# Kernel optimization log

Measured on AMD Instinct MI355X. Metric: run time of the kernel, lower is better.

Reference implementation:

```python
import jax, jax.numpy as jnp
import numpy as np

TOP_K = 2

def _sparse_moe(x, gate_w, w1, w2, w3):
    # x: [b, S, D] -> per-token top-k routed SwiGLU experts (Mixtral style)
    D = x.shape[-1]
    E = gate_w.shape[1]
    t = x.reshape(-1, D)                      # [T, D] tokens
    logits = t @ gate_w                       # [T, E]
    probs = jax.nn.softmax(logits, axis=-1)
    topw, topi = jax.lax.top_k(probs, TOP_K)  # [T, k]
    topw = topw / jnp.sum(topw, axis=-1, keepdims=True)
    out = jnp.zeros_like(t)
    for e in range(E):  # small fixed expert loop
        w_e = jnp.sum(jnp.where(topi == e, topw, 0.0), axis=-1)  # [T]
        h = jax.nn.silu(t @ w1[e]) * (t @ w3[e])                 # [T, F]
        out = out + (h @ w2[e]) * w_e[:, None]
    return out.reshape(x.shape)

def setup_inputs() -> dict:
    key = jax.random.key(0)
    ks = jax.random.split(key, 5)
    B, S, D, F, E = 4, 512, 1024, 4096, 8
    sc = 0.02
    return {
        "data": jax.random.normal(ks[0], (B, S, D), jnp.float32),
        "gate_w": jax.random.normal(ks[1], (D, E), jnp.float32) * sc,
        "w1": jax.random.normal(ks[2], (E, D, F), jnp.float32) * sc,
        "w2": jax.random.normal(ks[3], (E, F, D), jnp.float32) * sc,
        "w3": jax.random.normal(ks[4], (E, D, F), jnp.float32) * sc,
    }

def reference(data, gate_w, w1, w2, w3):
    # FeedForward._mixlora_forward: slice batch per lora config, run MoE,
    # combine with index_add_ (disjoint ranges covering the batch).
    B = data.shape[0]
    splits = [(0, B // 2), (B // 2, B)]  # two lora_batch_data_config_ entries
    final = jnp.zeros_like(data)
    for s, e in splits:
        y = _sparse_moe(data[s:e], gate_w, w1, w2, w3)
        final = final.at[jnp.arange(s, e)].add(y)  # index_add_ combine
    return final
```

## Files before the change

kernel.cpp:

```cpp
#include <hip/hip_runtime.h>
#include <hip/hip_bf16.h>
#include <math.h>

#define D_DIM 1024
#define F_DIM 4096
#define N_EXP 8

typedef __attribute__((ext_vector_type(4))) float f32x4;
typedef __attribute__((ext_vector_type(8))) short bf16x8;

__device__ __forceinline__ unsigned short f2bf(float f) {
    union { float f; unsigned int u; } v; v.f = f;
    unsigned int r = v.u + 0x7fffu + ((v.u >> 16) & 1u);
    return (unsigned short)(r >> 16);
}

#define GLDS16(g, l) __builtin_amdgcn_global_load_lds( \
    (const __attribute__((address_space(1))) void*)(g), \
    (__attribute__((address_space(3))) void*)(l), 16, 0, 0)

#define WAIT12_BAR asm volatile("s_waitcnt vmcnt(12)\ns_barrier" ::: "memory")
#define WAIT9_BAR  asm volatile("s_waitcnt vmcnt(9)\ns_barrier" ::: "memory")
#define BAR        asm volatile("s_barrier" ::: "memory")
#define DRAIN      asm volatile("s_waitcnt vmcnt(0)" ::: "memory")

__global__ void cast_x_kernel(const float* __restrict__ x, unsigned short* __restrict__ xb, int n4) {
    int i = blockIdx.x * blockDim.x + threadIdx.x;
    if (i >= n4) return;
    float4 v = ((const float4*)x)[i];
    unsigned int lo = (unsigned int)f2bf(v.x) | ((unsigned int)f2bf(v.y) << 16);
    unsigned int hi = (unsigned int)f2bf(v.z) | ((unsigned int)f2bf(v.w) << 16);
    ((uint2*)xb)[i] = make_uint2(lo, hi);
}

__global__ __launch_bounds__(256) void transpose_cast_kernel(
    const float* __restrict__ in, unsigned short* __restrict__ out, int R, int C) {
    __shared__ float tile[64][65];
    int e = blockIdx.x & 7;
    const float* inp = in + (size_t)e * R * C;
    unsigned short* outp = out + (size_t)e * R * C;
    int r0 = blockIdx.y * 64, c0 = (blockIdx.x >> 3) * 64;
    int tid = threadIdx.x;
    int tr = tid >> 4, tc = (tid & 15) * 4;
#pragma unroll
    for (int i = 0; i < 4; i++) {
        float4 v = *(const float4*)(inp + (size_t)(r0 + tr + i * 16) * C + c0 + tc);
        tile[tr + i * 16][tc + 0] = v.x;
        tile[tr + i * 16][tc + 1] = v.y;
        tile[tr + i * 16][tc + 2] = v.z;
        tile[tr + i * 16][tc + 3] = v.w;
    }
    __syncthreads();
    int wc = tid >> 4, wr = (tid & 15) * 4;
#pragma unroll
    for (int i = 0; i < 4; i++) {
        int c = wc + i * 16;
        ushort4 o;
        o.x = f2bf(tile[wr + 0][c]);
        o.y = f2bf(tile[wr + 1][c]);
        o.z = f2bf(tile[wr + 2][c]);
        o.w = f2bf(tile[wr + 3][c]);
        *(ushort4*)(outp + (size_t)(c0 + c) * R + r0 + wr) = o;
    }
}

__global__ void gate_kernel(const float* __restrict__ x, const float* __restrict__ gw,
                            int* __restrict__ counts, int* __restrict__ perm,
                            float* __restrict__ wts, int* __restrict__ islot, int T) {
    int wid = threadIdx.x >> 6, lane = threadIdx.x & 63;
    int token = blockIdx.x * 4 + wid;
    if (token >= T) return;
    float acc[N_EXP];
#pragma unroll
    for (int e = 0; e < N_EXP; e++) acc[e] = 0.f;
    const float* xr = x + (size_t)token * D_DIM;
    for (int i = 0; i < D_DIM / 64; i++) {
        int d = lane + 64 * i;
        float v = xr[d];
#pragma unroll
        for (int e = 0; e < N_EXP; e++) acc[e] += v * gw[d * N_EXP + e];
    }
#pragma unroll
    for (int off = 32; off >= 1; off >>= 1) {
#pragma unroll
        for (int e = 0; e < N_EXP; e++) acc[e] += __shfl_xor(acc[e], off, 64);
    }
    if (lane == 0) {
        float m = acc[0];
#pragma unroll
        for (int e = 1; e < N_EXP; e++) m = fmaxf(m, acc[e]);
        float p[N_EXP];
#pragma unroll
        for (int e = 0; e < N_EXP; e++) p[e] = expf(acc[e] - m);
        int a = 0;
        for (int e = 1; e < N_EXP; e++) if (p[e] > p[a]) a = e;
        int b = (a == 0) ? 1 : 0;
        for (int e = 0; e < N_EXP; e++) if (e != a && p[e] > p[b]) b = e;
        float s = p[a] + p[b];
        int pa = atomicAdd(&counts[a], 1);
        perm[(size_t)a * T + pa] = token; wts[(size_t)a * T + pa] = p[a] / s;
        int pb = atomicAdd(&counts[b], 1);
        perm[(size_t)b * T + pb] = token; wts[(size_t)b * T + pb] = p[b] / s;
        islot[2 * token + 0] = a * T + pa;
        islot[2 * token + 1] = b * T + pb;
    }
}

__global__ void offsets_kernel(const int* __restrict__ counts, int* __restrict__ offs) {
    if (threadIdx.x == 0 && blockIdx.x == 0) {
        int s = 0;
        for (int e = 0; e < N_EXP; e++) { offs[e] = s; s += counts[e]; }
        offs[N_EXP] = s;
    }
}

__global__ __launch_bounds__(256, 4) void gemm1_kernel(
    const unsigned short* __restrict__ xb, const unsigned short* __restrict__ w1t,
    const unsigned short* __restrict__ w3t, const int* __restrict__ counts,
    const int* __restrict__ offs, const int* __restrict__ perm,
    unsigned short* __restrict__ hbuf, int T)
{
    int bid = blockIdx.x;
    int s  = bid & 7;
    int rt = (bid >> 3) & 15;
    int ce = ((bid >> 7) << 3) | s;
    int e  = ce & 7;
    int ct = ce >> 3;
    int n_e = counts[e];
    int row0 = rt * 128;
    if (row0 >= n_e) return;
    int c0 = ct * 64;
    const unsigned short* w1e = w1t + (size_t)e * F_DIM * D_DIM;
    const unsigned short* w3e = w3t + (size_t)e * F_DIM * D_DIM;
    __shared__ __attribute__((aligned(16))) unsigned short As[4][4096];
    __shared__ __attribute__((aligned(16))) unsigned short B1s[4][2048];
    __shared__ __attribute__((aligned(16))) unsigned short B3s[4][2048];
    int tid = threadIdx.x;
    int wid = tid >> 6, lane = tid & 63;
    int wm = wid >> 1, wn = wid & 1;
    int q = lane >> 4, ln = lane & 15;

    int sr = tid >> 2, sc = tid & 3;
    int q0 = sc ^ ((sr >> 1) & 3);
    int tok0 = perm[(size_t)e * T + min(row0 + sr, n_e - 1)];
    int tok1 = perm[(size_t)e * T + min(row0 + sr + 64, n_e - 1)];
    const unsigned short* ag0 = xb + (size_t)tok0 * D_DIM + q0 * 8;
    const unsigned short* ag1 = xb + (size_t)tok1 * D_DIM + q0 * 8;
    const unsigned short* b1g = w1e + (size_t)(c0 + sr) * D_DIM + q0 * 8;
    const unsigned short* b3g = w3e + (size_t)(c0 + sr) * D_DIM + q0 * 8;
    int wo = wid * 512;

    int a_off[4], b_off[2];
#pragma unroll
    for (int i = 0; i < 4; i++) {
        int m = wm * 64 + i * 16 + ln;
        a_off[i] = m * 32 + (q ^ ((m >> 1) & 3)) * 8;
    }
#pragma unroll
    for (int j = 0; j < 2; j++) {
        int n = wn * 32 + j * 16 + ln;
        b_off[j] = n * 32 + (q ^ ((n >> 1) & 3)) * 8;
    }

    f32x4 acc1[4][2], acc3[4][2];
#pragma unroll
    for (int i = 0; i < 4; i++)
#pragma unroll
        for (int j = 0; j < 2; j++) {
            acc1[i][j] = (f32x4){0.f, 0.f, 0.f, 0.f};
            acc3[i][j] = (f32x4){0.f, 0.f, 0.f, 0.f};
        }

#define ISSUE1(B, K) do { \
    GLDS16(ag0 + (K), &As[B][wo]); \
    GLDS16(ag1 + (K), &As[B][wo + 2048]); \
    GLDS16(b1g + (K), &B1s[B][wo]); \
    GLDS16(b3g + (K), &B3s[B][wo]); } while (0)

#define COMPUTE1(B) do { \
    bf16x8 af[4]; \
    _Pragma("unroll") for (int i = 0; i < 4; i++) af[i] = *(const bf16x8*)&As[B][a_off[i]]; \
    _Pragma("unroll") for (int j = 0; j < 2; j++) { \
        bf16x8 b1f = *(const bf16x8*)&B1s[B][b_off[j]]; \
        bf16x8 b3f = *(const bf16x8*)&B3s[B][b_off[j]]; \
        _Pragma("unroll") for (int i = 0; i < 4; i++) { \
            acc1[i][j] = __builtin_amdgcn_mfma_f32_16x16x32_bf16(af[i], b1f, acc1[i][j], 0, 0, 0); \
            acc3[i][j] = __builtin_amdgcn_mfma_f32_16x16x32_bf16(af[i], b3f, acc3[i][j], 0, 0, 0); \
        } \
    } } while (0)

    ISSUE1(0, 0);
    ISSUE1(1, 32);
    ISSUE1(2, 64);
    for (int it = 0; it < 32; it += 4) {
        int k3 = it + 3, k4 = it + 4, k5 = it + 5, k6 = it + 6;
        ISSUE1(3, (k3 < 32) ? k3 * 32 : 0);
        WAIT12_BAR; COMPUTE1(0); BAR;
        ISSUE1(0, (k4 < 32) ? k4 * 32 : 0);
        WAIT12_BAR; COMPUTE1(1); BAR;
        ISSUE1(1, (k5 < 32) ? k5 * 32 : 0);
        WAIT12_BAR; COMPUTE1(2); BAR;
        ISSUE1(2, (k6 < 32) ? k6 * 32 : 0);
        WAIT12_BAR; COMPUTE1(3); BAR;
    }
    DRAIN;

    int hb = offs[e];
#pragma unroll
    for (int i = 0; i < 4; i++) {
#pragma unroll
        for (int r = 0; r < 4; r++) {
            int grow = row0 + wm * 64 + i * 16 + q * 4 + r;
            if (grow < n_e) {
                size_t hrow = (size_t)(hb + grow) * F_DIM;
#pragma unroll
                for (int j = 0; j < 2; j++) {
                    int col = c0 + wn * 32 + j * 16 + ln;
                    float p1 = acc1[i][j][r];
                    float p3 = acc3[i][j][r];
                    float h = (p1 / (1.f + expf(-p1))) * p3;
                    hbuf[hrow + col] = f2bf(h);
                }
            }
        }
    }
}

__global__ __launch_bounds__(256, 4) void gemm2_kernel(
    const unsigned short* __restrict__ hbuf, const unsigned short* __restrict__ w2t,
    const int* __restrict__ counts, const int* __restrict__ offs,
    const float* __restrict__ wts, float* __restrict__ obuf, int T)
{
    int bid = blockIdx.x;
    int s  = bid & 7;
    int rt = (bid >> 3) & 15;
    int ce = ((bid >> 7) << 3) | s;
    int e  = ce & 7;
    int ct = ce >> 3;
    int n_e = counts[e];
    int row0 = rt * 128;
    if (row0 >= n_e) return;
    int c0 = ct * 64;
    const unsigned short* w2e = w2t + (size_t)e * D_DIM * F_DIM;
    __shared__ __attribute__((aligned(16))) unsigned short As[4][4096];
    __shared__ __attribute__((aligned(16))) unsigned short Bs[4][2048];
    int tid = threadIdx.x;
    int wid = tid >> 6, lane = tid & 63;
    int wm = wid >> 1, wn = wid & 1;
    int q = lane >> 4, ln = lane & 15;
    int hb = offs[e];

    int sr = tid >> 2, sc = tid & 3;
    int q0 = sc ^ ((sr >> 1) & 3);
    int ar0 = hb + min(row0 + sr, n_e - 1);
    int ar1 = hb + min(row0 + sr + 64, n_e - 1);
    const unsigned short* ag0 = hbuf + (size_t)ar0 * F_DIM + q0 * 8;
    const unsigned short* ag1 = hbuf + (size_t)ar1 * F_DIM + q0 * 8;
    const unsigned short* bg  = w2e + (size_t)(c0 + sr) * F_DIM + q0 * 8;
    int wo = wid * 512;

    int a_off[4], b_off[2];
#pragma unroll
    for (int i = 0; i < 4; i++) {
        int m = wm * 64 + i * 16 + ln;
        a_off[i] = m * 32 + (q ^ ((m >> 1) & 3)) * 8;
    }
#pragma unroll
    for (int j = 0; j < 2; j++) {
        int n = wn * 32 + j * 16 + ln;
        b_off[j] = n * 32 + (q ^ ((n >> 1) & 3)) * 8;
    }

    f32x4 acc[4][2];
#pragma unroll
    for (int i = 0; i < 4; i++)
#pragma unroll
        for (int j = 0; j < 2; j++) acc[i][j] = (f32x4){0.f, 0.f, 0.f, 0.f};

#define ISSUE2(B, K) do { \
    GLDS16(ag0 + (K), &As[B][wo]); \
    GLDS16(ag1 + (K), &As[B][wo + 2048]); \
    GLDS16(bg + (K), &Bs[B][wo]); } while (0)

#define COMPUTE2(B) do { \
    bf16x8 af[4]; \
    _Pragma("unroll") for (int i = 0; i < 4; i++) af[i] = *(const bf16x8*)&As[B][a_off[i]]; \
    _Pragma("unroll") for (int j = 0; j < 2; j++) { \
        bf16x8 bf = *(const bf16x8*)&Bs[B][b_off[j]]; \
        _Pragma("unroll") for (int i = 0; i < 4; i++) \
            acc[i][j] = __builtin_amdgcn_mfma_f32_16x16x32_bf16(af[i], bf, acc[i][j], 0, 0, 0); \
    } } while (0)

    ISSUE2(0, 0);
    ISSUE2(1, 32);
    ISSUE2(2, 64);
    for (int it = 0; it < 128; it += 4) {
        int k3 = it + 3, k4 = it + 4, k5 = it + 5, k6 = it + 6;
        ISSUE2(3, (k3 < 128) ? k3 * 32 : 0);
        WAIT9_BAR; COMPUTE2(0); BAR;
        ISSUE2(0, (k4 < 128) ? k4 * 32 : 0);
        WAIT9_BAR; COMPUTE2(1); BAR;
        ISSUE2(1, (k5 < 128) ? k5 * 32 : 0);
        WAIT9_BAR; COMPUTE2(2); BAR;
        ISSUE2(2, (k6 < 128) ? k6 * 32 : 0);
        WAIT9_BAR; COMPUTE2(3); BAR;
    }
    DRAIN;

#pragma unroll
    for (int i = 0; i < 4; i++) {
#pragma unroll
        for (int r = 0; r < 4; r++) {
            int grow = row0 + wm * 64 + i * 16 + q * 4 + r;
            if (grow < n_e) {
                float w = wts[(size_t)e * T + grow];
                float* orow = obuf + (size_t)(hb + grow) * D_DIM;
#pragma unroll
                for (int j = 0; j < 2; j++) {
                    int col = c0 + wn * 32 + j * 16 + ln;
                    orow[col] = acc[i][j][r] * w;
                }
            }
        }
    }
}

__global__ void combine_kernel(const float* __restrict__ obuf, const int* __restrict__ islot,
                               const int* __restrict__ offs, float* __restrict__ out, int T) {
    int idx = blockIdx.x * 256 + threadIdx.x;
    int n4 = T * (D_DIM / 4);
    if (idx >= n4) return;
    int t = idx / (D_DIM / 4);
    int c4 = idx - t * (D_DIM / 4);
    int v0 = islot[2 * t], v1 = islot[2 * t + 1];
    int e0 = v0 / T, e1 = v1 / T;
    int s0 = offs[e0] + (v0 - e0 * T);
    int s1 = offs[e1] + (v1 - e1 * T);
    float4 a = ((const float4*)obuf)[(size_t)s0 * (D_DIM / 4) + c4];
    float4 b = ((const float4*)obuf)[(size_t)s1 * (D_DIM / 4) + c4];
    float4 o; o.x = a.x + b.x; o.y = a.y + b.y; o.z = a.z + b.z; o.w = a.w + b.w;
    ((float4*)out)[idx] = o;
}

extern "C" void kernel_launch(void* const* d_in, const int* in_sizes, int n_in,
                              void* d_out, int out_size, void* d_ws, size_t ws_size,
                              hipStream_t stream) {
    const float* x  = (const float*)d_in[0];
    const float* gw = (const float*)d_in[1];
    const float* w1 = (const float*)d_in[2];
    const float* w2 = (const float*)d_in[3];
    const float* w3 = (const float*)d_in[4];
    float* out = (float*)d_out;
    int T = in_sizes[0] / D_DIM;

    char* ws = (char*)d_ws;
    size_t off = 0;
    unsigned short* xb = (unsigned short*)(ws + off); off += (size_t)T * D_DIM * 2;
    int* counts = (int*)(ws + off); off += 256;
    int* offs   = (int*)(ws + off); off += 256;
    int* perm   = (int*)(ws + off); off += (size_t)N_EXP * T * 4;
    float* wts  = (float*)(ws + off); off += (size_t)N_EXP * T * 4;
    int* islot  = (int*)(ws + off); off += (size_t)2 * T * 4;
    unsigned short* hbuf = (unsigned short*)(ws + off); off += (size_t)2 * T * F_DIM * 2;
    unsigned short* w1t  = (unsigned short*)(ws + off); off += (size_t)N_EXP * D_DIM * F_DIM * 2;
    unsigned short* w3t  = (unsigned short*)(ws + off); off += (size_t)N_EXP * D_DIM * F_DIM * 2;
    unsigned short* w2t  = w1t;
    float* obuf = (float*)w3t;

    hipMemsetAsync(counts, 0, 256, stream);

    int n4 = T * D_DIM / 4;
    cast_x_kernel<<<(n4 + 255) / 256, 256, 0, stream>>>(x, xb, n4);
    gate_kernel<<<T / 4, 256, 0, stream>>>(x, gw, counts, perm, wts, islot, T);
    offsets_kernel<<<1, 64, 0, stream>>>(counts, offs);

    dim3 gt13((F_DIM / 64) * N_EXP, D_DIM / 64);
    transpose_cast_kernel<<<gt13, 256, 0, stream>>>(w1, w1t, D_DIM, F_DIM);
    transpose_cast_kernel<<<gt13, 256, 0, stream>>>(w3, w3t, D_DIM, F_DIM);

    gemm1_kernel<<<(F_DIM / 64) * N_EXP * 16, 256, 0, stream>>>(
        xb, w1t, w3t, counts, offs, perm, hbuf, T);

    dim3 gt2((D_DIM / 64) * N_EXP, F_DIM / 64);
    transpose_cast_kernel<<<gt2, 256, 0, stream>>>(w2, w2t, F_DIM, D_DIM);

    gemm2_kernel<<<(D_DIM / 64) * N_EXP * 16, 256, 0, stream>>>(
        hbuf, w2t, counts, offs, wts, obuf, T);

    combine_kernel<<<(T * D_DIM / 4 + 255) / 256, 256, 0, stream>>>(obuf, islot, offs, out, T);
}
```

Baseline: 761.3 us.

## Widen expert GEMM tiles to 128x128 with double-buffered LDS pipeline

Measured after the change: 721.4 us. -5.2%, faster.

```diff
diff --git a/kernel.cpp b/kernel.cpp
--- a/kernel.cpp
+++ b/kernel.cpp
@@ -19,10 +19,10 @@
     (const __attribute__((address_space(1))) void*)(g), \
     (__attribute__((address_space(3))) void*)(l), 16, 0, 0)
 
-#define WAIT12_BAR asm volatile("s_waitcnt vmcnt(12)\ns_barrier" ::: "memory")
-#define WAIT9_BAR  asm volatile("s_waitcnt vmcnt(9)\ns_barrier" ::: "memory")
-#define BAR        asm volatile("s_barrier" ::: "memory")
-#define DRAIN      asm volatile("s_waitcnt vmcnt(0)" ::: "memory")
+#define WAIT6_BAR asm volatile("s_waitcnt vmcnt(6)\ns_barrier" ::: "memory")
+#define WAIT4_BAR asm volatile("s_waitcnt vmcnt(4)\ns_barrier" ::: "memory")
+#define BAR       asm volatile("s_barrier" ::: "memory")
+#define DRAIN     asm volatile("s_waitcnt vmcnt(0)" ::: "memory")
 
 __global__ void cast_x_kernel(const float* __restrict__ x, unsigned short* __restrict__ xb, int n4) {
     int i = blockIdx.x * blockDim.x + threadIdx.x;
@@ -114,7 +114,7 @@
     }
 }
 
-__global__ __launch_bounds__(256, 4) void gemm1_kernel(
+__global__ __launch_bounds__(256, 2) void gemm1_kernel(
     const unsigned short* __restrict__ xb, const unsigned short* __restrict__ w1t,
     const unsigned short* __restrict__ w3t, const int* __restrict__ counts,
     const int* __restrict__ offs, const int* __restrict__ perm,
@@ -129,12 +129,12 @@
     int n_e = counts[e];
     int row0 = rt * 128;
     if (row0 >= n_e) return;
-    int c0 = ct * 64;
+    int c0 = ct * 128;
     const unsigned short* w1e = w1t + (size_t)e * F_DIM * D_DIM;
     const unsigned short* w3e = w3t + (size_t)e * F_DIM * D_DIM;
-    __shared__ __attribute__((aligned(16))) unsigned short As[4][4096];
-    __shared__ __attribute__((aligned(16))) unsigned short B1s[4][2048];
-    __shared__ __attribute__((aligned(16))) unsigned short B3s[4][2048];
+    __shared__ __attribute__((aligned(16))) unsigned short As[2][4096];
+    __shared__ __attribute__((aligned(16))) unsigned short B1s[2][4096];
+    __shared__ __attribute__((aligned(16))) unsigned short B3s[2][4096];
     int tid = threadIdx.x;
     int wid = tid >> 6, lane = tid & 63;
     int wm = wid >> 1, wn = wid & 1;
@@ -146,27 +146,29 @@
     int tok1 = perm[(size_t)e * T + min(row0 + sr + 64, n_e - 1)];
     const unsigned short* ag0 = xb + (size_t)tok0 * D_DIM + q0 * 8;
     const unsigned short* ag1 = xb + (size_t)tok1 * D_DIM + q0 * 8;
-    const unsigned short* b1g = w1e + (size_t)(c0 + sr) * D_DIM + q0 * 8;
-    const unsigned short* b3g = w3e + (size_t)(c0 + sr) * D_DIM + q0 * 8;
+    const unsigned short* b1g0 = w1e + (size_t)(c0 + sr) * D_DIM + q0 * 8;
+    const unsigned short* b1g1 = w1e + (size_t)(c0 + sr + 64) * D_DIM + q0 * 8;
+    const unsigned short* b3g0 = w3e + (size_t)(c0 + sr) * D_DIM + q0 * 8;
+    const unsigned short* b3g1 = w3e + (size_t)(c0 + sr + 64) * D_DIM + q0 * 8;
     int wo = wid * 512;
 
-    int a_off[4], b_off[2];
+    int a_off[4], b_off[4];
 #pragma unroll
     for (int i = 0; i < 4; i++) {
         int m = wm * 64 + i * 16 + ln;
         a_off[i] = m * 32 + (q ^ ((m >> 1) & 3)) * 8;
     }
 #pragma unroll
-    for (int j = 0; j < 2; j++) {
-        int n = wn * 32 + j * 16 + ln;
+    for (int j = 0; j < 4; j++) {
+        int n = wn * 64 + j * 16 + ln;
         b_off[j] = n * 32 + (q ^ ((n >> 1) & 3)) * 8;
     }
 
-    f32x4 acc1[4][2], acc3[4][2];
+    f32x4 acc1[4][4], acc3[4][4];
 #pragma unroll
     for (int i = 0; i < 4; i++)
 #pragma unroll
-        for (int j = 0; j < 2; j++) {
+        for (int j = 0; j < 4; j++) {
             acc1[i][j] = (f32x4){0.f, 0.f, 0.f, 0.f};
             acc3[i][j] = (f32x4){0.f, 0.f, 0.f, 0.f};
         }
@@ -174,13 +176,15 @@
 #define ISSUE1(B, K) do { \
     GLDS16(ag0 + (K), &As[B][wo]); \
     GLDS16(ag1 + (K), &As[B][wo + 2048]); \
-    GLDS16(b1g + (K), &B1s[B][wo]); \
-    GLDS16(b3g + (K), &B3s[B][wo]); } while (0)
+    GLDS16(b1g0 + (K), &B1s[B][wo]); \
+    GLDS16(b1g1 + (K), &B1s[B][wo + 2048]); \
+    GLDS16(b3g0 + (K), &B3s[B][wo]); \
+    GLDS16(b3g1 + (K), &B3s[B][wo + 2048]); } while (0)
 
 #define COMPUTE1(B) do { \
     bf16x8 af[4]; \
     _Pragma("unroll") for (int i = 0; i < 4; i++) af[i] = *(const bf16x8*)&As[B][a_off[i]]; \
-    _Pragma("unroll") for (int j = 0; j < 2; j++) { \
+    _Pragma("unroll") for (int j = 0; j < 4; j++) { \
         bf16x8 b1f = *(const bf16x8*)&B1s[B][b_off[j]]; \
         bf16x8 b3f = *(const bf16x8*)&B3s[B][b_off[j]]; \
         _Pragma("unroll") for (int i = 0; i < 4; i++) { \
@@ -190,18 +194,17 @@
     } } while (0)
 
     ISSUE1(0, 0);
-    ISSUE1(1, 32);
-    ISSUE1(2, 64);
-    for (int it = 0; it < 32; it += 4) {
-        int k3 = it + 3, k4 = it + 4, k5 = it + 5, k6 = it + 6;
-        ISSUE1(3, (k3 < 32) ? k3 * 32 : 0);
-        WAIT12_BAR; COMPUTE1(0); BAR;
-        ISSUE1(0, (k4 < 32) ? k4 * 32 : 0);
-        WAIT12_BAR; COMPUTE1(1); BAR;
-        ISSUE1(1, (k5 < 32) ? k5 * 32 : 0);
-        WAIT12_BAR; COMPUTE1(2); BAR;
-        ISSUE1(2, (k6 < 32) ? k6 * 32 : 0);
-        WAIT12_BAR; COMPUTE1(3); BAR;
+    for (int it = 0; it < 32; it += 2) {
+        int kn1 = (it + 1) * 32;
+        ISSUE1(1, kn1);
+        WAIT6_BAR;
+        COMPUTE1(0);
+        BAR;
+        int kn2 = (it + 2 < 32) ? (it + 2) * 32 : 0;
+        ISSUE1(0, kn2);
+        WAIT6_BAR;
+        COMPUTE1(1);
+        BAR;
     }
     DRAIN;
 
@@ -214,8 +217,8 @@
             if (grow < n_e) {
                 size_t hrow = (size_t)(hb + grow) * F_DIM;
 #pragma unroll
-                for (int j = 0; j < 2; j++) {
-                    int col = c0 + wn * 32 + j * 16 + ln;
+                for (int j = 0; j < 4; j++) {
+                    int col = c0 + wn * 64 + j * 16 + ln;
                     float p1 = acc1[i][j][r];
                     float p3 = acc3[i][j][r];
                     float h = (p1 / (1.f + expf(-p1))) * p3;
@@ -226,7 +229,7 @@
     }
 }
 
-__global__ __launch_bounds__(256, 4) void gemm2_kernel(
+__global__ __launch_bounds__(256, 2) void gemm2_kernel(
     const unsigned short* __restrict__ hbuf, const unsigned short* __restrict__ w2t,
     const int* __restrict__ counts, const int* __restrict__ offs,
     const float* __restrict__ wts, float* __restrict__ obuf, int T)
@@ -240,10 +243,10 @@
     int n_e = counts[e];
     int row0 = rt * 128;
     if (row0 >= n_e) return;
-    int c0 = ct * 64;
+    int c0 = ct * 128;
     const unsigned short* w2e = w2t + (size_t)e * D_DIM * F_DIM;
-    __shared__ __attribute__((aligned(16))) unsigned short As[4][4096];
-    __shared__ __attribute__((aligned(16))) unsigned short Bs[4][2048];
+    __shared__ __attribute__((aligned(16))) unsigned short As[2][4096];
+    __shared__ __attribute__((aligned(16))) unsigned short Bs[2][4096];
     int tid = threadIdx.x;
     int wid = tid >> 6, lane = tid & 63;
     int wm = wid >> 1, wn = wid & 1;
@@ -256,54 +259,55 @@
     int ar1 = hb + min(row0 + sr + 64, n_e - 1);
     const unsigned short* ag0 = hbuf + (size_t)ar0 * F_DIM + q0 * 8;
     const unsigned short* ag1 = hbuf + (size_t)ar1 * F_DIM + q0 * 8;
-    const unsigned short* bg  = w2e + (size_t)(c0 + sr) * F_DIM + q0 * 8;
+    const unsigned short* bg0 = w2e + (size_t)(c0 + sr) * F_DIM + q0 * 8;
+    const unsigned short* bg1 = w2e + (size_t)(c0 + sr + 64) * F_DIM + q0 * 8;
     int wo = wid * 512;
 
-    int a_off[4], b_off[2];
+    int a_off[4], b_off[4];
 #pragma unroll
     for (int i = 0; i < 4; i++) {
         int m = wm * 64 + i * 16 + ln;
         a_off[i] = m * 32 + (q ^ ((m >> 1) & 3)) * 8;
     }
 #pragma unroll
-    for (int j = 0; j < 2; j++) {
-        int n = wn * 32 + j * 16 + ln;
+    for (int j = 0; j < 4; j++) {
+        int n = wn * 64 + j * 16 + ln;
         b_off[j] = n * 32 + (q ^ ((n >> 1) & 3)) * 8;
     }
 
-    f32x4 acc[4][2];
+    f32x4 acc[4][4];
 #pragma unroll
     for (int i = 0; i < 4; i++)
 #pragma unroll
-        for (int j = 0; j < 2; j++) acc[i][j] = (f32x4){0.f, 0.f, 0.f, 0.f};
+        for (int j = 0; j < 4; j++) acc[i][j] = (f32x4){0.f, 0.f, 0.f, 0.f};
 
 #define ISSUE2(B, K) do { \
     GLDS16(ag0 + (K), &As[B][wo]); \
     GLDS16(ag1 + (K), &As[B][wo + 2048]); \
-    GLDS16(bg + (K), &Bs[B][wo]); } while (0)
+    GLDS16(bg0 + (K), &Bs[B][wo]); \
+    GLDS16(bg1 + (K), &Bs[B][wo + 2048]); } while (0)
 
 #define COMPUTE2(B) do { \
     bf16x8 af[4]; \
     _Pragma("unroll") for (int i = 0; i < 4; i++) af[i] = *(const bf16x8*)&As[B][a_off[i]]; \
-    _Pragma("unroll") for (int j = 0; j < 2; j++) { \
+    _Pragma("unroll") for (int j = 0; j < 4; j++) { \
         bf16x8 bf = *(const bf16x8*)&Bs[B][b_off[j]]; \
         _Pragma("unroll") for (int i = 0; i < 4; i++) \
             acc[i][j] = __builtin_amdgcn_mfma_f32_16x16x32_bf16(af[i], bf, acc[i][j], 0, 0, 0); \
     } } while (0)
 
     ISSUE2(0, 0);
-    ISSUE2(1, 32);
-    ISSUE2(2, 64);
-    for (int it = 0; it < 128; it += 4) {
-        int k3 = it + 3, k4 = it + 4, k5 = it + 5, k6 = it + 6;
-        ISSUE2(3, (k3 < 128) ? k3 * 32 : 0);
-        WAIT9_BAR; COMPUTE2(0); BAR;
-        ISSUE2(0, (k4 < 128) ? k4 * 32 : 0);
-        WAIT9_BAR; COMPUTE2(1); BAR;
-        ISSUE2(1, (k5 < 128) ? k5 * 32 : 0);
-        WAIT9_BAR; COMPUTE2(2); BAR;
-        ISSUE2(2, (k6 < 128) ? k6 * 32 : 0);
-        WAIT9_BAR; COMPUTE2(3); BAR;
+    for (int it = 0; it < 128; it += 2) {
+        int kn1 = (it + 1) * 32;
+        ISSUE2(1, kn1);
+        WAIT4_BAR;
+        COMPUTE2(0);
+        BAR;
+        int kn2 = (it + 2 < 128) ? (it + 2) * 32 : 0;
+        ISSUE2(0, kn2);
+        WAIT4_BAR;
+        COMPUTE2(1);
+        BAR;
     }
     DRAIN;
 
@@ -316,8 +320,8 @@
                 float w = wts[(size_t)e * T + grow];
                 float* orow = obuf + (size_t)(hb + grow) * D_DIM;
 #pragma unroll
-                for (int j = 0; j < 2; j++) {
-                    int col = c0 + wn * 32 + j * 16 + ln;
+                for (int j = 0; j < 4; j++) {
+                    int col = c0 + wn * 64 + j * 16 + ln;
                     orow[col] = acc[i][j][r] * w;
                 }
             }
@@ -378,13 +382,13 @@
     transpose_cast_kernel<<<gt13, 256, 0, stream>>>(w1, w1t, D_DIM, F_DIM);
     transpose_cast_kernel<<<gt13, 256, 0, stream>>>(w3, w3t, D_DIM, F_DIM);
 
-    gemm1_kernel<<<(F_DIM / 64) * N_EXP * 16, 256, 0, stream>>>(
+    gemm1_kernel<<<(F_DIM / 128) * N_EXP * 16, 256, 0, stream>>>(
         xb, w1t, w3t, counts, offs, perm, hbuf, T);
 
     dim3 gt2((D_DIM / 64) * N_EXP, F_DIM / 64);
     transpose_cast_kernel<<<gt2, 256, 0, stream>>>(w2, w2t, F_DIM, D_DIM);
 
-    gemm2_kernel<<<(D_DIM / 64) * N_EXP * 16, 256, 0, stream>>>(
+    gemm2_kernel<<<(D_DIM / 128) * N_EXP * 16, 256, 0, stream>>>(
         hbuf, w2t, counts, offs, wts, obuf, T);
 
     combine_kernel<<<(T * D_DIM / 4 + 255) / 256, 256, 0, stream>>>(obuf, islot, offs, out, T);
```
